# Optimization experiments

Hardware: AMD Instinct MI355X
Metric: run time of the kernel (lower is better)

## Reference

```python
import jax, jax.numpy as jnp
import numpy as np

VOCAB = 32000
D_TOTAL = 1024          # GRU hidden size
D_COMP = D_TOTAL // 2   # per real/imag embedding features
B, T = 8, 2048
LN_EPS = 1e-6           # flax LayerNorm default


def setup_inputs() -> dict:
    key = jax.random.key(0)
    ks = jax.random.split(key, 12)
    s_emb = 1.0 / np.sqrt(D_COMP)
    s_w = 1.0 / np.sqrt(2 * D_TOTAL)
    return {
        "token_ids": jax.random.randint(ks[0], (B, T), 0, VOCAB),
        "emb_r": jax.random.normal(ks[1], (VOCAB, D_COMP), jnp.float32) * s_emb,
        "emb_i": jax.random.normal(ks[2], (VOCAB, D_COMP), jnp.float32) * s_emb,
        "W_r": jax.random.normal(ks[3], (2 * D_TOTAL, D_TOTAL), jnp.float32) * s_w,
        "b_r": jnp.zeros((D_TOTAL,), jnp.float32),
        "W_u": jax.random.normal(ks[4], (2 * D_TOTAL, D_TOTAL), jnp.float32) * s_w,
        "b_u": jnp.zeros((D_TOTAL,), jnp.float32),
        "W_c": jax.random.normal(ks[5], (2 * D_TOTAL, D_TOTAL), jnp.float32) * s_w,
        "b_c": jnp.zeros((D_TOTAL,), jnp.float32),
        "ln_r_scale": jnp.ones((D_COMP,), jnp.float32),
        "ln_r_bias": jnp.zeros((D_COMP,), jnp.float32),
        "ln_i_scale": jnp.ones((D_COMP,), jnp.float32),
        "ln_i_bias": jnp.zeros((D_COMP,), jnp.float32),
    }


def _layernorm(x, scale, bias):
    mu = jnp.mean(x, axis=-1, keepdims=True)
    var = jnp.mean(jnp.square(x - mu), axis=-1, keepdims=True)
    return (x - mu) * jax.lax.rsqrt(var + LN_EPS) * scale + bias


def _forward(token_ids, emb_r, emb_i, W_r, b_r, W_u, b_u, W_c, b_c,
             ln_r_scale, ln_r_bias, ln_i_scale, ln_i_bias):
    # Complex embedding -> concat real/imag: [B, T, D_TOTAL]
    xs = jnp.concatenate([emb_r[token_ids], emb_i[token_ids]], axis=-1)
    xs_t = jnp.swapaxes(xs, 0, 1)  # [T, B, D_TOTAL] for scan over time

    def step(h, x_t):
        xh = jnp.concatenate([x_t, h], axis=-1)              # [B, 2D]
        r = jax.nn.sigmoid(xh @ W_r + b_r)
        u = jax.nn.sigmoid(xh @ W_u + b_u)
        c_in = jnp.concatenate([x_t, r * h], axis=-1)
        c = jnp.tanh(c_in @ W_c + b_c)
        h_new = (1.0 - u) * h + u * c
        return h_new, h_new

    h0 = jnp.zeros((token_ids.shape[0], D_TOTAL), xs.dtype)
    _, hs = jax.lax.scan(step, h0, xs_t)                      # [T, B, D]
    hs = jnp.swapaxes(hs, 0, 1)                               # [B, T, D]
    h_r, h_i = jnp.split(hs, 2, axis=-1)
    return (_layernorm(h_r, ln_r_scale, ln_r_bias),
            _layernorm(h_i, ln_i_scale, ln_i_bias))


def reference(token_ids, emb_r, emb_i, W_r, b_r, W_u, b_u, W_c, b_c,
              ln_r_scale, ln_r_bias, ln_i_scale, ln_i_bias):
    return _forward(token_ids, emb_r, emb_i, W_r, b_r, W_u, b_u, W_c, b_c,
                    ln_r_scale, ln_r_bias, ln_i_scale, ln_i_bias)
```

## Files before the change

kernel.cpp:

```cpp
#include <hip/hip_runtime.h>
#include <hip/hip_bf16.h>

#define B_   8
#define T_   2048
#define OUT1_OFF 8388608ull

typedef unsigned short u16;
typedef unsigned int   u32;
typedef unsigned long long u64;

__device__ __forceinline__ u16 f2bf(float f) {
  u32 u = __builtin_bit_cast(u32, f);
  u32 r = (u + 0x7fffu + ((u >> 16) & 1u)) >> 16;
  return (u16)r;
}
__device__ __forceinline__ float bf2f(u16 s) {
  u32 u = ((u32)s) << 16;
  return __builtin_bit_cast(float, u);
}
__device__ __forceinline__ u64 ald64(const u64* p) {
  return __hip_atomic_load(p, __ATOMIC_RELAXED, __HIP_MEMORY_SCOPE_AGENT);
}
__device__ __forceinline__ void ast64(u64* p, u64 v) {
  __hip_atomic_store(p, v, __ATOMIC_RELAXED, __HIP_MEMORY_SCOPE_AGENT);
}

__global__ void k_init(u64* recs) {
  int i = blockIdx.x * 256 + threadIdx.x;
  __hip_atomic_store(&recs[i], 0ull, __ATOMIC_RELAXED, __HIP_MEMORY_SCOPE_AGENT);
}

__global__ __launch_bounds__(256) void k_prep(const float* __restrict__ Wr,
                                              const float* __restrict__ Wu,
                                              const float* __restrict__ Wc,
                                              u16* __restrict__ WT,
                                              u16* __restrict__ WTh) {
  __shared__ float tile[32][33];
  int bid = blockIdx.x;
  int g = bid >> 11;
  int rest = bid & 2047;
  int kt = rest >> 5;
  int jt = rest & 31;
  const float* W = (g == 0) ? Wr : ((g == 1) ? Wu : Wc);
  int tid = threadIdx.x;
  int r = tid >> 3, c4 = (tid & 7) * 4;
  const float4 v = *(const float4*)&W[(size_t)(kt * 32 + r) * 1024 + jt * 32 + c4];
  tile[r][c4 + 0] = v.x; tile[r][c4 + 1] = v.y;
  tile[r][c4 + 2] = v.z; tile[r][c4 + 3] = v.w;
  __syncthreads();
  int n = g * 1024 + jt * 32 + r;
  ushort4 o;
  o.x = f2bf(tile[c4 + 0][r]); o.y = f2bf(tile[c4 + 1][r]);
  o.z = f2bf(tile[c4 + 2][r]); o.w = f2bf(tile[c4 + 3][r]);
  if (kt < 32) {
    int k = kt * 32 + c4;
    *(ushort4*)&WT[(size_t)n * 1024 + k] = o;
  } else {
    int k = (kt - 32) * 32 + c4;
    *(ushort4*)&WTh[(size_t)n * 1024 + k] = o;
  }
}

__global__ __launch_bounds__(256) void k_gather(const int* __restrict__ tok,
                                                const float* __restrict__ er,
                                                const float* __restrict__ ei,
                                                u16* __restrict__ XS) {
  int row = blockIdx.x * 2 + (threadIdx.x >> 7);
  int lt = threadIdx.x & 127;
  int tk = tok[row];
  int c0 = lt * 8;
  const float* p = (c0 < 512) ? (er + (size_t)tk * 512 + c0)
                              : (ei + (size_t)tk * 512 + (c0 - 512));
  float4 v1 = *(const float4*)p;
  float4 v2 = *(const float4*)(p + 4);
  uint4 o;
  o.x = (u32)f2bf(v1.x) | ((u32)f2bf(v1.y) << 16);
  o.y = (u32)f2bf(v1.z) | ((u32)f2bf(v1.w) << 16);
  o.z = (u32)f2bf(v2.x) | ((u32)f2bf(v2.y) << 16);
  o.w = (u32)f2bf(v2.z) | ((u32)f2bf(v2.w) << 16);
  *(uint4*)&XS[(size_t)row * 1024 + c0] = o;
}

typedef __attribute__((ext_vector_type(8))) __bf16 bf16x8;
typedef __attribute__((ext_vector_type(4))) float f32x4;

__device__ __forceinline__ void gload16(const void* g, void* l) {
  __builtin_amdgcn_global_load_lds((const __attribute__((address_space(1))) void*)g,
                                   (__attribute__((address_space(3))) void*)l, 16, 0, 0);
}

__global__ __launch_bounds__(256) void k_gemm(const u16* __restrict__ XS,
                                              const u16* __restrict__ WT,
                                              u16* __restrict__ XW) {
  __shared__ u16 As[128 * 32];
  __shared__ u16 Bs[128 * 32];
  int bid = blockIdx.x;
  int m0 = (bid & 127) * 128;
  int n0 = (bid >> 7) * 128;
  int tid = threadIdx.x;
  int wave = tid >> 6, lane = tid & 63;
  int wm = wave >> 1, wn = wave & 1;
  f32x4 acc[4][4] = {};
  int lr = lane & 15, lk = (lane >> 4) * 8;
  int srow = lane >> 2, sc8 = (lane & 3) * 8;
  for (int k0 = 0; k0 < 1024; k0 += 32) {
#pragma unroll
    for (int q = 0; q < 2; ++q) {
      int rbase = wave * 32 + q * 16;
      gload16(XS + (size_t)(m0 + rbase + srow) * 1024 + k0 + sc8, &As[rbase * 32]);
      gload16(WT + (size_t)(n0 + rbase + srow) * 1024 + k0 + sc8, &Bs[rbase * 32]);
    }
    __syncthreads();
    bf16x8 a[4], b[4];
#pragma unroll
    for (int mi = 0; mi < 4; ++mi) a[mi] = *(const bf16x8*)&As[(wm * 64 + mi * 16 + lr) * 32 + lk];
#pragma unroll
    for (int ni = 0; ni < 4; ++ni) b[ni] = *(const bf16x8*)&Bs[(wn * 64 + ni * 16 + lr) * 32 + lk];
#pragma unroll
    for (int mi = 0; mi < 4; ++mi)
#pragma unroll
      for (int ni = 0; ni < 4; ++ni)
        acc[mi][ni] = __builtin_amdgcn_mfma_f32_16x16x32_bf16(a[mi], b[ni], acc[mi][ni], 0, 0, 0);
    __syncthreads();
  }
#pragma unroll
  for (int mi = 0; mi < 4; ++mi)
#pragma unroll
    for (int ni = 0; ni < 4; ++ni) {
      int col = n0 + wn * 64 + ni * 16 + lr;
#pragma unroll
      for (int r = 0; r < 4; ++r) {
        int row = m0 + wm * 64 + mi * 16 + (lane >> 4) * 4 + r;
        XW[(size_t)row * 3072 + col] = f2bf(acc[mi][ni][r]);
      }
    }
}

template <int N>
__device__ __forceinline__ float foldreduce(float (&p)[N], int lane) {
#pragma unroll
  for (int s = 0; (1 << s) < N; ++s) {
    const int m = 1 << s;
    const int bit = (lane >> s) & 1;
#pragma unroll
    for (int i = 0; i < (N >> (s + 1)); ++i) {
      float lo = p[2 * i], hi = p[2 * i + 1];
      float mine = bit ? hi : lo;
      float send = bit ? lo : hi;
      p[i] = mine + __shfl_xor(send, m, 64);
    }
  }
  float v = p[0];
#pragma unroll
  for (int s = 0; s < 6; ++s)
    if ((1 << s) >= N) v += __shfl_xor(v, 1 << s, 64);
  return v;
}

__global__ __launch_bounds__(512, 1) void k_gru(const u16* __restrict__ WTh,
                                                const float* __restrict__ br,
                                                const float* __restrict__ bu,
                                                const float* __restrict__ bc,
                                                const u16* __restrict__ XW,
                                                u64* __restrict__ hrec,
                                                u64* __restrict__ rrec,
                                                float* __restrict__ out) {
  __shared__ float h_l[1024];
  __shared__ float u_l[32];
  __shared__ float hown_l[32];

  const int tid = threadIdx.x;
  const int L = tid & 63;
  const int w = tid >> 6;
  const int isl = blockIdx.x >> 5;
  const int wg = blockIdx.x & 31;
  const int j0 = wg * 32;

  u32 wA[8][8];
#pragma unroll
  for (int i = 0; i < 8; ++i) {
    int p = w * 8 + i;
    const u16* wr = WTh + (size_t)((p >> 5) * 1024 + j0 + (p & 31)) * 1024;
#pragma unroll
    for (int j2 = 0; j2 < 8; ++j2) {
      u32 a = wr[128 * j2 + L];
      u32 b = wr[128 * j2 + 64 + L];
      wA[i][j2] = a | (b << 16);
    }
  }
  u32 wB[4][8];
#pragma unroll
  for (int i = 0; i < 4; ++i) {
    const u16* wr = WTh + (size_t)(2048 + j0 + w * 4 + i) * 1024;
#pragma unroll
    for (int j2 = 0; j2 < 8; ++j2) {
      u32 a = wr[128 * j2 + L];
      u32 b = wr[128 * j2 + 64 + L];
      wB[i][j2] = a | (b << 16);
    }
  }

  float biasA = 0.f, bcB = 0.f;
  if (L < 8) {
    int p = w * 8 + L;
    biasA = ((p >= 32) ? bu : br)[j0 + (p & 31)];
  }
  if (L < 4) bcB = bc[j0 + w * 4 + L];
  if (tid < 32) hown_l[tid] = 0.f;

  u64* hr = hrec + (size_t)isl * 512;
  u64* rr = rrec + (size_t)isl * 512;

  __syncthreads();

  for (int t = 0; t < T_; ++t) {
    const size_t xrow = ((size_t)isl * T_ + t) * 3072;
    float xwA = 0.f, xwB = 0.f;
    if (L < 8) {
      int p = w * 8 + L;
      xwA = bf2f(XW[xrow + (p >> 5) * 1024 + j0 + (p & 31)]);
    }
    if (L < 4) xwB = bf2f(XW[xrow + 2048 + j0 + w * 4 + L]);

    u64 hv = ald64(&hr[tid]);
    while ((u32)(hv >> 32) < (u32)t) hv = ald64(&hr[tid]);
    float2 hst;
    hst.x = bf2f((u16)hv);
    hst.y = bf2f((u16)(hv >> 16));
    ((float2*)h_l)[tid] = hst;
    __syncthreads();

    float hreg[16];
#pragma unroll
    for (int j = 0; j < 16; ++j) hreg[j] = h_l[64 * j + L];
    float acc[8];
#pragma unroll
    for (int i = 0; i < 8; ++i) {
      float s = 0.f;
#pragma unroll
      for (int j2 = 0; j2 < 8; ++j2) {
        u32 wp = wA[i][j2];
        s += __builtin_bit_cast(float, wp << 16) * hreg[2 * j2]
           + __builtin_bit_cast(float, wp & 0xffff0000u) * hreg[2 * j2 + 1];
      }
      acc[i] = s;
    }
    float dA = foldreduce<8>(acc, L);
    float sg = 1.f / (1.f + __expf(-(dA + xwA + biasA)));
    float rhv = 0.f;
    if (L < 8 && w < 4) rhv = sg * hown_l[w * 8 + L];
    float rhp = __shfl_xor(rhv, 1, 64);
    if (w < 4 && L < 8 && (L & 1) == 0) {
      int p = w * 8 + L;
      u64 x = ((u64)(u32)(t + 1) << 32) |
              (u64)((u32)f2bf(rhv) | ((u32)f2bf(rhp) << 16));
      ast64(&rr[(j0 + p) >> 1], x);
    }
    if (L < 8 && w >= 4) u_l[w * 8 + L - 32] = sg;
    __syncthreads();

    u64 rv = ald64(&rr[tid]);
    while ((u32)(rv >> 32) < (u32)(t + 1)) rv = ald64(&rr[tid]);
    float2 rst;
    rst.x = bf2f((u16)rv);
    rst.y = bf2f((u16)(rv >> 16));
    ((float2*)h_l)[tid] = rst;
    __syncthreads();

    float rreg[16];
#pragma unroll
    for (int j = 0; j < 16; ++j) rreg[j] = h_l[64 * j + L];
    float accB[4];
#pragma unroll
    for (int i = 0; i < 4; ++i) {
      float s = 0.f;
#pragma unroll
      for (int j2 = 0; j2 < 8; ++j2) {
        u32 wp = wB[i][j2];
        s += __builtin_bit_cast(float, wp << 16) * rreg[2 * j2]
           + __builtin_bit_cast(float, wp & 0xffff0000u) * rreg[2 * j2 + 1];
      }
      accB[i] = s;
    }
    float dB = foldreduce<4>(accB, L);
    float hn = 0.f;
    if (L < 4) {
      int c = w * 4 + L;
      float pre = dB + xwB + bcB;
      float ax = fabsf(pre);
      float e = __expf(-2.f * ax);
      float cv = copysignf((1.f - e) / (1.f + e), pre);
      float uu = u_l[c];
      hn = (1.f - uu) * hown_l[c] + uu * cv;
      hown_l[c] = hn;
      int j = j0 + c;
      size_t orow = (size_t)isl * T_ + t;
      if (j < 512) out[orow * 512 + j] = hn;
      else out[OUT1_OFF + orow * 512 + (j - 512)] = hn;
    }
    float hp = __shfl_xor(hn, 1, 64);
    if (L < 4 && (L & 1) == 0) {
      int j = j0 + w * 4 + L;
      u64 x = ((u64)(u32)(t + 1) << 32) |
              (u64)((u32)f2bf(hn) | ((u32)f2bf(hp) << 16));
      ast64(&hr[j >> 1], x);
    }
    __syncthreads();
  }
}

__global__ __launch_bounds__(256) void k_ln(float* __restrict__ out,
                                            const float* __restrict__ sr,
                                            const float* __restrict__ brr,
                                            const float* __restrict__ si,
                                            const float* __restrict__ bii) {
  int row = blockIdx.x * 4 + (threadIdx.x >> 6);
  int lane = threadIdx.x & 63;
  float* p = out + (size_t)row * 512;
  float4 v1 = ((const float4*)p)[lane];
  float4 v2 = ((const float4*)p)[64 + lane];
  float s1 = v1.x + v1.y + v1.z + v1.w + v2.x + v2.y + v2.z + v2.w;
  float s2 = v1.x * v1.x + v1.y * v1.y + v1.z * v1.z + v1.w * v1.w +
             v2.x * v2.x + v2.y * v2.y + v2.z * v2.z + v2.w * v2.w;
#pragma unroll
  for (int m = 1; m < 64; m <<= 1) { s1 += __shfl_xor(s1, m, 64); s2 += __shfl_xor(s2, m, 64); }
  float mean = s1 * (1.f / 512.f);
  float var = s2 * (1.f / 512.f) - mean * mean;
  float inv = rsqrtf(var + 1e-6f);
  bool hi2 = row >= 16384;
  const float* sc = hi2 ? si : sr;
  const float* bs = hi2 ? bii : brr;
  float4 g1 = ((const float4*)sc)[lane], g2 = ((const float4*)sc)[64 + lane];
  float4 b1 = ((const float4*)bs)[lane], b2 = ((const float4*)bs)[64 + lane];
  v1.x = (v1.x - mean) * inv * g1.x + b1.x;
  v1.y = (v1.y - mean) * inv * g1.y + b1.y;
  v1.z = (v1.z - mean) * inv * g1.z + b1.z;
  v1.w = (v1.w - mean) * inv * g1.w + b1.w;
  v2.x = (v2.x - mean) * inv * g2.x + b2.x;
  v2.y = (v2.y - mean) * inv * g2.y + b2.y;
  v2.z = (v2.z - mean) * inv * g2.z + b2.z;
  v2.w = (v2.w - mean) * inv * g2.w + b2.w;
  ((float4*)p)[lane] = v1;
  ((float4*)p)[64 + lane] = v2;
}

extern "C" void kernel_launch(void* const* d_in, const int* in_sizes, int n_in,
                              void* d_out, int out_size, void* d_ws, size_t ws_size,
                              hipStream_t stream) {
  const int*   tok   = (const int*)d_in[0];
  const float* emb_r = (const float*)d_in[1];
  const float* emb_i = (const float*)d_in[2];
  const float* Wr    = (const float*)d_in[3];
  const float* br    = (const float*)d_in[4];
  const float* Wu    = (const float*)d_in[5];
  const float* bu    = (const float*)d_in[6];
  const float* Wc    = (const float*)d_in[7];
  const float* bc    = (const float*)d_in[8];
  const float* lnrs  = (const float*)d_in[9];
  const float* lnrb  = (const float*)d_in[10];
  const float* lnis  = (const float*)d_in[11];
  const float* lnib  = (const float*)d_in[12];
  float* out = (float*)d_out;
  char* ws = (char*)d_ws;

  u16*   XS    = (u16*)(ws);
  u16*   WT    = (u16*)(ws + 33554432);
  u16*   WTh   = (u16*)(ws + 39845888);
  u16*   XW    = (u16*)(ws + 46137344);
  u64*   hrec  = (u64*)(ws + 146800640);
  u64*   rrec  = (u64*)(ws + 146833408);

  k_init<<<32, 256, 0, stream>>>(hrec);
  k_prep<<<6144, 256, 0, stream>>>(Wr, Wu, Wc, WT, WTh);
  k_gather<<<8192, 256, 0, stream>>>(tok, emb_r, emb_i, XS);
  k_gemm<<<3072, 256, 0, stream>>>(XS, WT, XW);
  k_gru<<<256, 512, 0, stream>>>(WTh, br, bu, bc, XW, hrec, rrec, out);
  k_ln<<<8192, 256, 0, stream>>>(out, lnrs, lnrb, lnis, lnib);
}
```

Baseline: 7.666 ms.

## Use packed fp16 dot2 for recurrent GEMV and drop extra block barriers

Recurrent weights are now stored as fp16 and the h/r·W products use the packed fdot2 instruction on fp16 pairs, replacing bf16 unpacking and scalar FMAs. The published state is packed as fp16 and staged in LDS as raw u32 words. Row assignment is changed so each wave owns 4 output columns for both reset and update gates. This lets the update gate and own hidden state stay in registers and be exchanged by shuffles, which removes the shared u_l/hown_l arrays and two of the four __syncthreads per timestep. The fp16 range and precision replace bf16 on the recurrent path, and separate h/r LDS buffers avoid the write-after-read hazard that the removed barriers used to cover.

Measured after the change: 10.01 ms. +30.6%, slower.

```diff
diff --git a/kernel.cpp b/kernel.cpp
--- a/kernel.cpp
+++ b/kernel.cpp
@@ -8,6 +8,7 @@
 typedef unsigned short u16;
 typedef unsigned int   u32;
 typedef unsigned long long u64;
+typedef __attribute__((ext_vector_type(2))) _Float16 f16x2;
 
 __device__ __forceinline__ u16 f2bf(float f) {
   u32 u = __builtin_bit_cast(u32, f);
@@ -18,11 +19,24 @@
   u32 u = ((u32)s) << 16;
   return __builtin_bit_cast(float, u);
 }
+__device__ __forceinline__ u16 f2h(float f) {
+  _Float16 h = (_Float16)f;
+  return __builtin_bit_cast(u16, h);
+}
 __device__ __forceinline__ u64 ald64(const u64* p) {
   return __hip_atomic_load(p, __ATOMIC_RELAXED, __HIP_MEMORY_SCOPE_AGENT);
 }
 __device__ __forceinline__ void ast64(u64* p, u64 v) {
   __hip_atomic_store(p, v, __ATOMIC_RELAXED, __HIP_MEMORY_SCOPE_AGENT);
+}
+__device__ __forceinline__ float dot2(u32 w, u32 h, float c) {
+#if defined(__has_builtin) && __has_builtin(__builtin_amdgcn_fdot2)
+  return __builtin_amdgcn_fdot2(__builtin_bit_cast(f16x2, w),
+                                __builtin_bit_cast(f16x2, h), c, false);
+#else
+  f16x2 a = __builtin_bit_cast(f16x2, w), b = __builtin_bit_cast(f16x2, h);
+  return c + (float)a.x * (float)b.x + (float)a.y * (float)b.y;
+#endif
 }
 
 __global__ void k_init(u64* recs) {
@@ -49,14 +63,17 @@
   tile[r][c4 + 2] = v.z; tile[r][c4 + 3] = v.w;
   __syncthreads();
   int n = g * 1024 + jt * 32 + r;
-  ushort4 o;
-  o.x = f2bf(tile[c4 + 0][r]); o.y = f2bf(tile[c4 + 1][r]);
-  o.z = f2bf(tile[c4 + 2][r]); o.w = f2bf(tile[c4 + 3][r]);
   if (kt < 32) {
     int k = kt * 32 + c4;
+    ushort4 o;
+    o.x = f2bf(tile[c4 + 0][r]); o.y = f2bf(tile[c4 + 1][r]);
+    o.z = f2bf(tile[c4 + 2][r]); o.w = f2bf(tile[c4 + 3][r]);
     *(ushort4*)&WT[(size_t)n * 1024 + k] = o;
   } else {
     int k = (kt - 32) * 32 + c4;
+    ushort4 o;
+    o.x = f2h(tile[c4 + 0][r]); o.y = f2h(tile[c4 + 1][r]);
+    o.z = f2h(tile[c4 + 2][r]); o.w = f2h(tile[c4 + 3][r]);
     *(ushort4*)&WTh[(size_t)n * 1024 + k] = o;
   }
 }
@@ -165,9 +182,8 @@
                                                 u64* __restrict__ hrec,
                                                 u64* __restrict__ rrec,
                                                 float* __restrict__ out) {
-  __shared__ float h_l[1024];
-  __shared__ float u_l[32];
-  __shared__ float hown_l[32];
+  __shared__ u32 h_pk[512];
+  __shared__ u32 r_pk[512];
 
   const int tid = threadIdx.x;
   const int L = tid & 63;
@@ -178,134 +194,96 @@
 
   u32 wA[8][8];
 #pragma unroll
-  for (int i = 0; i < 8; ++i) {
-    int p = w * 8 + i;
-    const u16* wr = WTh + (size_t)((p >> 5) * 1024 + j0 + (p & 31)) * 1024;
-#pragma unroll
-    for (int j2 = 0; j2 < 8; ++j2) {
-      u32 a = wr[128 * j2 + L];
-      u32 b = wr[128 * j2 + 64 + L];
-      wA[i][j2] = a | (b << 16);
-    }
+  for (int s = 0; s < 8; ++s) {
+    int g = s >> 2, i = s & 3;
+    const u32* wr = (const u32*)(WTh + (size_t)(g * 1024 + j0 + w * 4 + i) * 1024);
+#pragma unroll
+    for (int j2 = 0; j2 < 8; ++j2) wA[s][j2] = wr[64 * j2 + L];
   }
   u32 wB[4][8];
 #pragma unroll
   for (int i = 0; i < 4; ++i) {
-    const u16* wr = WTh + (size_t)(2048 + j0 + w * 4 + i) * 1024;
-#pragma unroll
-    for (int j2 = 0; j2 < 8; ++j2) {
-      u32 a = wr[128 * j2 + L];
-      u32 b = wr[128 * j2 + 64 + L];
-      wB[i][j2] = a | (b << 16);
-    }
-  }
-
-  float biasA = 0.f, bcB = 0.f;
-  if (L < 8) {
-    int p = w * 8 + L;
-    biasA = ((p >= 32) ? bu : br)[j0 + (p & 31)];
-  }
-  if (L < 4) bcB = bc[j0 + w * 4 + L];
-  if (tid < 32) hown_l[tid] = 0.f;
+    const u32* wr = (const u32*)(WTh + (size_t)(2048 + j0 + w * 4 + i) * 1024);
+#pragma unroll
+    for (int j2 = 0; j2 < 8; ++j2) wB[i][j2] = wr[64 * j2 + L];
+  }
+
+  const float biasA = (((L >> 2) & 1) ? bu : br)[j0 + w * 4 + (L & 3)];
+  const float bcB = bc[j0 + w * 4 + (L & 3)];
+  float hown = 0.f;
+  float sgA = 0.f;
 
   u64* hr = hrec + (size_t)isl * 512;
   u64* rr = rrec + (size_t)isl * 512;
-
-  __syncthreads();
+  const int qpub = wg * 16 + w * 2 + ((L >> 1) & 1);
 
   for (int t = 0; t < T_; ++t) {
     const size_t xrow = ((size_t)isl * T_ + t) * 3072;
-    float xwA = 0.f, xwB = 0.f;
-    if (L < 8) {
-      int p = w * 8 + L;
-      xwA = bf2f(XW[xrow + (p >> 5) * 1024 + j0 + (p & 31)]);
-    }
-    if (L < 4) xwB = bf2f(XW[xrow + 2048 + j0 + w * 4 + L]);
+    float xwA = bf2f(XW[xrow + ((L >> 2) & 1) * 1024 + j0 + w * 4 + (L & 3)]);
+    float xwB = bf2f(XW[xrow + 2048 + j0 + w * 4 + (L & 3)]);
 
     u64 hv = ald64(&hr[tid]);
     while ((u32)(hv >> 32) < (u32)t) hv = ald64(&hr[tid]);
-    float2 hst;
-    hst.x = bf2f((u16)hv);
-    hst.y = bf2f((u16)(hv >> 16));
-    ((float2*)h_l)[tid] = hst;
+    h_pk[tid] = (u32)hv;
     __syncthreads();
 
-    float hreg[16];
-#pragma unroll
-    for (int j = 0; j < 16; ++j) hreg[j] = h_l[64 * j + L];
+    u32 hq[8];
+#pragma unroll
+    for (int j2 = 0; j2 < 8; ++j2) hq[j2] = h_pk[64 * j2 + L];
     float acc[8];
 #pragma unroll
-    for (int i = 0; i < 8; ++i) {
-      float s = 0.f;
-#pragma unroll
-      for (int j2 = 0; j2 < 8; ++j2) {
-        u32 wp = wA[i][j2];
-        s += __builtin_bit_cast(float, wp << 16) * hreg[2 * j2]
-           + __builtin_bit_cast(float, wp & 0xffff0000u) * hreg[2 * j2 + 1];
-      }
-      acc[i] = s;
+    for (int s = 0; s < 8; ++s) {
+      float a = 0.f;
+#pragma unroll
+      for (int j2 = 0; j2 < 8; ++j2) a = dot2(wA[s][j2], hq[j2], a);
+      acc[s] = a;
     }
     float dA = foldreduce<8>(acc, L);
-    float sg = 1.f / (1.f + __expf(-(dA + xwA + biasA)));
-    float rhv = 0.f;
-    if (L < 8 && w < 4) rhv = sg * hown_l[w * 8 + L];
-    float rhp = __shfl_xor(rhv, 1, 64);
-    if (w < 4 && L < 8 && (L & 1) == 0) {
-      int p = w * 8 + L;
+    sgA = 1.f / (1.f + __expf(-(dA + xwA + biasA)));
+    float rh = sgA * hown;
+    float rhp = __shfl_xor(rh, 1, 64);
+    if (L < 4 && (L & 1) == 0) {
       u64 x = ((u64)(u32)(t + 1) << 32) |
-              (u64)((u32)f2bf(rhv) | ((u32)f2bf(rhp) << 16));
-      ast64(&rr[(j0 + p) >> 1], x);
-    }
-    if (L < 8 && w >= 4) u_l[w * 8 + L - 32] = sg;
-    __syncthreads();
+              (u64)((u32)f2h(rh) | ((u32)f2h(rhp) << 16));
+      ast64(&rr[qpub], x);
+    }
 
     u64 rv = ald64(&rr[tid]);
     while ((u32)(rv >> 32) < (u32)(t + 1)) rv = ald64(&rr[tid]);
-    float2 rst;
-    rst.x = bf2f((u16)rv);
-    rst.y = bf2f((u16)(rv >> 16));
-    ((float2*)h_l)[tid] = rst;
+    r_pk[tid] = (u32)rv;
     __syncthreads();
 
-    float rreg[16];
-#pragma unroll
-    for (int j = 0; j < 16; ++j) rreg[j] = h_l[64 * j + L];
+    u32 rq[8];
+#pragma unroll
+    for (int j2 = 0; j2 < 8; ++j2) rq[j2] = r_pk[64 * j2 + L];
     float accB[4];
 #pragma unroll
     for (int i = 0; i < 4; ++i) {
-      float s = 0.f;
-#pragma unroll
-      for (int j2 = 0; j2 < 8; ++j2) {
-        u32 wp = wB[i][j2];
-        s += __builtin_bit_cast(float, wp << 16) * rreg[2 * j2]
-           + __builtin_bit_cast(float, wp & 0xffff0000u) * rreg[2 * j2 + 1];
-      }
-      accB[i] = s;
+      float a = 0.f;
+#pragma unroll
+      for (int j2 = 0; j2 < 8; ++j2) a = dot2(wB[i][j2], rq[j2], a);
+      accB[i] = a;
     }
     float dB = foldreduce<4>(accB, L);
-    float hn = 0.f;
+    float pre = dB + xwB + bcB;
+    float ax = fabsf(pre);
+    float e = __expf(-2.f * ax);
+    float cv = copysignf((1.f - e) / (1.f + e), pre);
+    float uu = __shfl_xor(sgA, 4, 64);
+    float hn = (1.f - uu) * hown + uu * cv;
+    if (L < 4) hown = hn;
+    float hp = __shfl_xor(hn, 1, 64);
+    if (L < 4 && (L & 1) == 0) {
+      u64 x = ((u64)(u32)(t + 1) << 32) |
+              (u64)((u32)f2h(hn) | ((u32)f2h(hp) << 16));
+      ast64(&hr[qpub], x);
+    }
     if (L < 4) {
-      int c = w * 4 + L;
-      float pre = dB + xwB + bcB;
-      float ax = fabsf(pre);
-      float e = __expf(-2.f * ax);
-      float cv = copysignf((1.f - e) / (1.f + e), pre);
-      float uu = u_l[c];
-      hn = (1.f - uu) * hown_l[c] + uu * cv;
-      hown_l[c] = hn;
-      int j = j0 + c;
+      int j = j0 + w * 4 + L;
       size_t orow = (size_t)isl * T_ + t;
       if (j < 512) out[orow * 512 + j] = hn;
       else out[OUT1_OFF + orow * 512 + (j - 512)] = hn;
     }
-    float hp = __shfl_xor(hn, 1, 64);
-    if (L < 4 && (L & 1) == 0) {
-      int j = j0 + w * 4 + L;
-      u64 x = ((u64)(u32)(t + 1) << 32) |
-              (u64)((u32)f2bf(hn) | ((u32)f2bf(hp) << 16));
-      ast64(&hr[j >> 1], x);
-    }
-    __syncthreads();
   }
 }
 
```
